# Kernel tuning notes

Hardware: AMD Instinct MI355X
Metric: run time of the kernel (lower is better)

## Reference

```python
import jax, jax.numpy as jnp
import numpy as np
import math

# dims
B, T, D = 2, 1024, 1024
HQ, HKV, KD, VD = 16, 4, 64, 64   # query heads, kv heads, key dim, value dim
G = HQ // HKV                      # query group size
E, TOPK, CAP_FRAC, HID = 8, 2, 0.5, 2048
BASE = 10000.0
EPS = 1e-6


def setup_inputs() -> dict:
    key = jax.random.key(0)
    ks = jax.random.split(key, 12)
    s = jnp.float32(0.02)
    return {
        'x': jax.random.normal(ks[0], (B, T, D), jnp.float32),
        'wq': jax.random.normal(ks[1], (D, KD * HQ), jnp.float32) * s,
        'wk': jax.random.normal(ks[2], (D, KD * HKV), jnp.float32) * s,
        'wv': jax.random.normal(ks[3], (D, VD * HKV), jnp.float32) * s,
        'wo': jax.random.normal(ks[4], (G * HKV * VD, D), jnp.float32) * s,
        'router_w': jax.random.normal(ks[5], (D, E), jnp.float32) * s,
        'router_b': jax.random.normal(ks[6], (E,), jnp.float32) * s,
        'w1': jax.random.normal(ks[7], (E, D, HID), jnp.float32) * s,
        'w2': jax.random.normal(ks[8], (E, D, HID), jnp.float32) * s,
        'w3': jax.random.normal(ks[9], (E, HID, D), jnp.float32) * s,
        'norm1_scale': jnp.ones((D,), jnp.float32),
        'norm2_scale': jnp.ones((D,), jnp.float32),
    }


def _rms(x, scale):
    return x * jax.lax.rsqrt(jnp.mean(x * x, axis=-1, keepdims=True) + EPS) * scale


def _rope(x):
    # x: (B, t, H, d); rotary per RotaryEmbedding: tile(ticks,(1,2)), neg-half rotation
    t, d = x.shape[1], x.shape[3]
    thetas = BASE ** (-jnp.arange(0, d, 2, dtype=jnp.float32) / d)
    ticks = jnp.outer(jnp.arange(t, dtype=jnp.float32), thetas)
    ticks = jnp.tile(ticks, (1, 2))[None, :, None, :]
    cos, sin = jnp.cos(ticks).astype(x.dtype), jnp.sin(ticks).astype(x.dtype)
    x1, x2 = jnp.split(x, 2, axis=-1)
    neg = jnp.concatenate([-x2, x1], axis=-1)
    return x * cos + neg * sin


def reference(x, wq, wk, wv, wo, router_w, router_b, w1, w2, w3, norm1_scale, norm2_scale):
    b, t, d = x.shape
    # ---- pre-norm grouped-query attention with rotary, causal ----
    h = _rms(x, norm1_scale)
    q = (h @ wq).reshape(b, t, HQ, KD)
    k = (h @ wk).reshape(b, t, HKV, KD)
    v = (h @ wv).reshape(b, t, HKV, VD)
    q = _rope(q)
    k = _rope(k)
    qg = q.reshape(b, t, HKV, G, KD)
    scores = jnp.einsum('bthgk,bshk->bhgts', qg, k) / jnp.sqrt(jnp.asarray(KD, x.dtype))
    causal = jnp.tril(jnp.ones((t, t), bool))
    scores = jnp.where(causal, scores, jnp.asarray(-1e9, scores.dtype))
    probs = jax.nn.softmax(scores, axis=-1)
    attn = jnp.einsum('bhgts,bshv->bthgv', probs, v).reshape(b, t, HQ * VD)
    x = x + attn @ wo
    # ---- pre-norm top-k MoE feed-forward (capacity-masked dispatch/combine) ----
    h2 = _rms(x, norm2_scale)
    xf = h2.reshape(b * t, d)
    logits = xf.astype(jnp.float32) @ router_w + router_b        # router in fp32
    gate, assign = jax.lax.top_k(logits, TOPK)                   # (N,k)
    gate = jax.nn.softmax(gate, axis=-1).astype(x.dtype)
    cap = math.floor(b * t * CAP_FRAC)
    onehot = jax.nn.one_hot(assign, E, dtype=jnp.float32)        # (N,k,E)
    pos = jnp.cumsum(jnp.cumsum(onehot, axis=0), axis=1).astype(jnp.int32)
    mask = onehot * (pos < cap)                                  # capacity mask
    token_mask = jnp.sum(mask, axis=-1)                          # (N,k)
    choices = jnp.sum(jax.nn.one_hot(pos, cap, dtype=jnp.float32) * mask[..., None], axis=1)  # (N,E,cap)
    choices = choices.transpose(1, 2, 0)                         # (E,cap,N)
    exp_idx = jnp.einsum('tke,e->tk', mask, jnp.arange(E, dtype=jnp.float32)).astype(jnp.int32)
    pos_idx = jnp.einsum('tke,tke->tk', mask, pos.astype(jnp.float32)).astype(jnp.int32)
    grouped = jnp.einsum('ect,tD->ecD', choices.astype(x.dtype), xf)  # dispatch: (E,cap,D)
    # gated FF per expert: act(w2(x) * w1(x)) @ w3
    hh = jax.nn.gelu(jnp.einsum('ecd,edh->ech', grouped, w2) * jnp.einsum('ecd,edh->ech', grouped, w1))
    eout = jnp.einsum('ech,ehd->ecd', hh, w3)                    # (E,cap,D)
    gathered = eout[exp_idx, pos_idx].reshape(b, t, TOPK, d)
    tm = token_mask.reshape(b, t, TOPK)
    moe = jnp.where(tm[..., None] != 0, gathered, h2[:, :, None, :])  # dropped tokens fall back to input
    moe = jnp.einsum('btkD,btk->btD', moe, gate.reshape(b, t, TOPK))
    return x + moe
```

## Files before the change

### kernel.cpp

```cpp
#include <hip/hip_runtime.h>
#include <math.h>

#define Dm 1024
#define Tn 1024
#define Bn 2
#define NTOK 2048
#define HQn 16
#define HKVn 4
#define KDn 64
#define VDn 64
#define Gn 4
#define NE 8
#define CAPn 1024
#define HIDn 2048
#define QKVS 1536

using frag_ab = __attribute__((ext_vector_type(8))) short;
using f32x4  = __attribute__((ext_vector_type(4))) float;

__device__ __forceinline__ unsigned short f2bf(float f) {
    union { float f; unsigned int u; } v; v.f = f;
    unsigned int r = v.u + 0x7FFFu + ((v.u >> 16) & 1u);
    return (unsigned short)(r >> 16);
}
__device__ __forceinline__ float bf2f(unsigned short b) {
    union { unsigned int u; float f; } v; v.u = ((unsigned int)b) << 16;
    return v.f;
}
__device__ __forceinline__ float gelu_fast(float y) {
    float z = 0.7978845608028654f * (y + 0.044715f * y * y * y);
    float az = fabsf(z);
    float t = __expf(-2.f * az);
    float th = (1.f - t) / (1.f + t);
    th = copysignf(th, z);
    return 0.5f * y * (1.f + th);
}

__global__ void rmsnorm_bf16_kernel(const float* __restrict__ x, const float* __restrict__ scale,
                                    unsigned short* __restrict__ out) {
    int row = blockIdx.x;
    const float* xr = x + (size_t)row * Dm;
    float ss = 0.f;
    for (int d = threadIdx.x; d < Dm; d += 256) { float v = xr[d]; ss += v * v; }
    __shared__ float red[256];
    red[threadIdx.x] = ss; __syncthreads();
    for (int s = 128; s > 0; s >>= 1) {
        if (threadIdx.x < s) red[threadIdx.x] += red[threadIdx.x + s];
        __syncthreads();
    }
    float inv = rsqrtf(red[0] * (1.f / Dm) + 1e-6f);
    for (int d = threadIdx.x; d < Dm; d += 256)
        out[(size_t)row * Dm + d] = f2bf(xr[d] * inv * scale[d]);
}

__global__ void rmsnorm_router_kernel(const float* __restrict__ x2, const float* __restrict__ scale,
                                      const float* __restrict__ rw, const float* __restrict__ rb,
                                      float* __restrict__ h2, int* __restrict__ assign,
                                      float* __restrict__ gate) {
    int row = blockIdx.x;
    const float* xr = x2 + (size_t)row * Dm;
    __shared__ float red[256];
    __shared__ float rowbuf[Dm];
    __shared__ float logits[NE];
    float v4[4]; float ss = 0.f;
    #pragma unroll
    for (int i = 0; i < 4; ++i) { v4[i] = xr[threadIdx.x + 256 * i]; ss += v4[i] * v4[i]; }
    red[threadIdx.x] = ss; __syncthreads();
    for (int s = 128; s > 0; s >>= 1) {
        if (threadIdx.x < s) red[threadIdx.x] += red[threadIdx.x + s];
        __syncthreads();
    }
    float inv = rsqrtf(red[0] * (1.f / Dm) + 1e-6f);
    #pragma unroll
    for (int i = 0; i < 4; ++i) {
        int d = threadIdx.x + 256 * i;
        float h = v4[i] * inv * scale[d];
        h2[(size_t)row * Dm + d] = h;
        rowbuf[d] = h;
    }
    __syncthreads();
    int e = threadIdx.x >> 5, lane32 = threadIdx.x & 31;
    float part = 0.f;
    for (int d = lane32; d < Dm; d += 32) part += rowbuf[d] * rw[(size_t)d * NE + e];
    for (int off = 16; off; off >>= 1) part += __shfl_down(part, off, 32);
    if (lane32 == 0) logits[e] = part + rb[e];
    __syncthreads();
    if (threadIdx.x == 0) {
        int i0 = 0; float m0 = logits[0];
        for (int i = 1; i < NE; ++i) if (logits[i] > m0) { m0 = logits[i]; i0 = i; }
        int i1 = -1; float m1 = -1e30f;
        for (int i = 0; i < NE; ++i) if (i != i0 && logits[i] > m1) { m1 = logits[i]; i1 = i; }
        float e1 = __expf(m1 - m0);
        float s = 1.f + e1;
        assign[row * 2] = i0; assign[row * 2 + 1] = i1;
        gate[row * 2] = 1.f / s; gate[row * 2 + 1] = e1 / s;
    }
}

__global__ void transpose_convert(const float* __restrict__ in, unsigned short* __restrict__ out,
                                  int R, int Ccols) {
    int e = blockIdx.z;
    in  += (size_t)e * R * Ccols;
    out += (size_t)e * R * Ccols;
    __shared__ float T[64][65];
    int tid = threadIdx.x;
    int r0 = blockIdx.y * 64, c0 = blockIdx.x * 64;
    #pragma unroll
    for (int rep = 0; rep < 4; ++rep) {
        int r = (tid >> 4) + rep * 16;
        int c = (tid & 15) * 4;
        float4 v = *(const float4*)(in + (size_t)(r0 + r) * Ccols + c0 + c);
        T[r][c] = v.x; T[r][c + 1] = v.y; T[r][c + 2] = v.z; T[r][c + 3] = v.w;
    }
    __syncthreads();
    #pragma unroll
    for (int rep = 0; rep < 4; ++rep) {
        int c = rep * 16 + (tid >> 4);
        int r = (tid & 15) * 4;
        unsigned long long pk = (unsigned long long)f2bf(T[r][c])
                              | ((unsigned long long)f2bf(T[r + 1][c]) << 16)
                              | ((unsigned long long)f2bf(T[r + 2][c]) << 32)
                              | ((unsigned long long)f2bf(T[r + 3][c]) << 48);
        *(unsigned long long*)(out + (size_t)(c0 + c) * R + r0 + r) = pk;
    }
}

template<int MODE>
__global__ __launch_bounds__(256) void mfma_gemm2(const unsigned short* __restrict__ A,
                                                  const unsigned short* __restrict__ Bt,
                                                  void* __restrict__ Cout,
                                                  const float* __restrict__ R,
                                                  int N, int K) {
    int m0 = blockIdx.y * 128, n0 = blockIdx.x * 128;
    __shared__ unsigned short As[128 * 32];
    __shared__ unsigned short Bs[128 * 32];
    int tid = threadIdx.x, wave = tid >> 6, lane = tid & 63;
    int quad = lane >> 4, r16 = lane & 15;
    int wm = wave & 1, wn = wave >> 1;
    f32x4 acc[4][4];
    #pragma unroll
    for (int mt = 0; mt < 4; ++mt)
        #pragma unroll
        for (int nt = 0; nt < 4; ++nt) acc[mt][nt] = (f32x4){0.f, 0.f, 0.f, 0.f};
    const size_t rs = (size_t)K * 2;
    const char* ga0 = (const char*)A  + (size_t)m0 * rs;
    const char* gb0 = (const char*)Bt + (size_t)n0 * rs;
    for (int kk = 0; kk < K; kk += 32) {
        __syncthreads();
        #pragma unroll
        for (int i = 0; i < 2; ++i) {
            int r = wave * 16 + i * 64 + (lane >> 2);
            size_t go = (size_t)r * rs + (size_t)kk * 2 + (lane & 3) * 16;
            int lofs = wave * 1024 + i * 4096;
            __builtin_amdgcn_global_load_lds(
                (const __attribute__((address_space(1))) void*)(ga0 + go),
                (__attribute__((address_space(3))) void*)((char*)As + lofs), 16, 0, 0);
            __builtin_amdgcn_global_load_lds(
                (const __attribute__((address_space(1))) void*)(gb0 + go),
                (__attribute__((address_space(3))) void*)((char*)Bs + lofs), 16, 0, 0);
        }
        __syncthreads();
        frag_ab a[4], b[4];
        #pragma unroll
        for (int t = 0; t < 4; ++t) {
            a[t] = *(const frag_ab*)((const char*)As + (wm * 64 + t * 16 + r16) * 64 + quad * 16);
            b[t] = *(const frag_ab*)((const char*)Bs + (wn * 64 + t * 16 + r16) * 64 + quad * 16);
        }
        #pragma unroll
        for (int mt = 0; mt < 4; ++mt)
            #pragma unroll
            for (int nt = 0; nt < 4; ++nt)
                acc[mt][nt] = __builtin_amdgcn_mfma_f32_16x16x32_bf16(a[mt], b[nt], acc[mt][nt], 0, 0, 0);
    }
    #pragma unroll
    for (int mt = 0; mt < 4; ++mt)
        #pragma unroll
        for (int nt = 0; nt < 4; ++nt)
            #pragma unroll
            for (int r = 0; r < 4; ++r) {
                int m = m0 + wm * 64 + mt * 16 + quad * 4 + r;
                int n = n0 + wn * 64 + nt * 16 + r16;
                size_t idx = (size_t)m * N + n;
                float v = acc[mt][nt][r];
                if (MODE == 0) ((unsigned short*)Cout)[idx] = f2bf(v);
                else           ((float*)Cout)[idx] = v + R[idx];
            }
}

__global__ void rope_bf16(unsigned short* __restrict__ p) {
    int idx = blockIdx.x * 256 + threadIdx.x;
    const int QC = NTOK * HQn * 32;
    int i, col, row; float scale;
    if (idx < QC) {
        i = idx & 31; int h = (idx >> 5) & 15; row = idx >> 9;
        col = h * 64 + i; scale = 0.18033688011112042f;
    } else {
        int r = idx - QC;
        i = r & 31; int h = (r >> 5) & 3; row = r >> 7;
        col = 1024 + h * 64 + i; scale = 1.f;
    }
    int t = row & (Tn - 1);
    size_t base = (size_t)row * QKVS + col;
    float theta = __expf(-(float)i * (1.f / 32.f) * 9.210340371976184f);
    float ang = (float)t * theta;
    float c = cosf(ang), s = sinf(ang);
    float x1 = bf2f(p[base]), x2 = bf2f(p[base + 32]);
    p[base]      = f2bf((x1 * c - x2 * s) * scale);
    p[base + 32] = f2bf((x2 * c + x1 * s) * scale);
}

__global__ __launch_bounds__(256) void mfma_attn(const unsigned short* __restrict__ qkv,
                                                 unsigned short* __restrict__ attnb) {
    __shared__ unsigned short lds[32768];
    unsigned short* Ps = lds;
    unsigned short* Ks = lds + 16384;
    unsigned short* Vt = lds + 24576;
    int tid = threadIdx.x, wave = tid >> 6, lane = tid & 63;
    int quad = lane >> 4, r16 = lane & 15;
    int tq0 = blockIdx.x * 128, h = blockIdx.y, b = blockIdx.z;
    int kvh = h >> 2;
    const size_t rowb = QKVS * 2;

    {
        const char* qb = (const char*)(qkv + (size_t)(b * Tn + tq0) * QKVS + h * 64);
        int rloc = lane >> 3, ch = (lane & 7) ^ rloc;
        #pragma unroll
        for (int i = 0; i < 4; ++i) {
            int r0 = wave * 8 + i * 32;
            __builtin_amdgcn_global_load_lds(
                (const __attribute__((address_space(1))) void*)(qb + (size_t)(r0 + rloc) * rowb + ch * 16),
                (__attribute__((address_space(3))) void*)((char*)Vt + r0 * 128), 16, 0, 0);
        }
    }
    __syncthreads();
    frag_ab qf[2][2];
    #pragma unroll
    for (int mt = 0; mt < 2; ++mt)
        #pragma unroll
        for (int ks = 0; ks < 2; ++ks) {
            int m = wave * 32 + mt * 16 + r16;
            int ch = (ks * 4 + quad) ^ (m & 7);
            qf[mt][ks] = *(const frag_ab*)((const char*)Vt + m * 128 + ch * 16);
        }

    float m_i[2][4], l_i[2][4];
    f32x4 O[2][4];
    #pragma unroll
    for (int mt = 0; mt < 2; ++mt) {
        #pragma unroll
        for (int r = 0; r < 4; ++r) { m_i[mt][r] = -1e30f; l_i[mt][r] = 0.f; }
        #pragma unroll
        for (int nt = 0; nt < 4; ++nt) O[mt][nt] = (f32x4){0.f, 0.f, 0.f, 0.f};
    }

    int nst = blockIdx.x + 1;
    for (int st = 0; st < nst; ++st) {
        int s0 = st * 128;
        __syncthreads();
        {
            const char* kb = (const char*)(qkv + (size_t)(b * Tn + s0) * QKVS + 1024 + kvh * 64);
            int rloc = lane >> 3, ch = (lane & 7) ^ rloc;
            #pragma unroll
            for (int i = 0; i < 4; ++i) {
                int r0 = wave * 8 + i * 32;
                __builtin_amdgcn_global_load_lds(
                    (const __attribute__((address_space(1))) void*)(kb + (size_t)(r0 + rloc) * rowb + ch * 16),
                    (__attribute__((address_space(3))) void*)((char*)Ks + r0 * 128), 16, 0, 0);
            }
        }
        {
            const unsigned short* vb = qkv + (size_t)(b * Tn + s0) * QKVS + 1280 + kvh * 64;
            int d4 = (tid & 15) * 4;
            #pragma unroll
            for (int pass = 0; pass < 4; ++pass) {
                int sl = 8 * wave + 2 * (lane >> 4) + pass * 32;
                ushort4 v0 = *(const ushort4*)(vb + (size_t)sl * QKVS + d4);
                ushort4 v1 = *(const ushort4*)(vb + (size_t)(sl + 1) * QKVS + d4);
                unsigned short a0[4] = {v0.x, v0.y, v0.z, v0.w};
                unsigned short a1[4] = {v1.x, v1.y, v1.z, v1.w};
                #pragma unroll
                for (int i = 0; i < 4; ++i) {
                    int d = d4 + i;
                    int col = (((sl >> 3) ^ (d & 15)) << 3) | (sl & 7);
                    *(unsigned int*)(Vt + d * 128 + col) =
                        (unsigned int)a0[i] | ((unsigned int)a1[i] << 16);
                }
            }
        }
        __syncthreads();
        f32x4 Sacc[2][8];
        #pragma unroll
        for (int mt = 0; mt < 2; ++mt)
            #pragma unroll
            for (int nt = 0; nt < 8; ++nt) Sacc[mt][nt] = (f32x4){0.f, 0.f, 0.f, 0.f};
        #pragma unroll
        for (int ks = 0; ks < 2; ++ks) {
            frag_ab kf[8];
            #pragma unroll
            for (int nt = 0; nt < 8; ++nt) {
                int n = nt * 16 + r16;
                int ch = (ks * 4 + quad) ^ (n & 7);
                kf[nt] = *(const frag_ab*)((const char*)Ks + n * 128 + ch * 16);
            }
            #pragma unroll
            for (int mt = 0; mt < 2; ++mt)
                #pragma unroll
                for (int nt = 0; nt < 8; ++nt)
                    Sacc[mt][nt] = __builtin_amdgcn_mfma_f32_16x16x32_bf16(qf[mt][ks], kf[nt], Sacc[mt][nt], 0, 0, 0);
        }
        if (st == nst - 1) {
            #pragma unroll
            for (int mt = 0; mt < 2; ++mt) {
                int trow = wave * 32 + mt * 16 + quad * 4;
                #pragma unroll
                for (int nt = 0; nt < 8; ++nt) {
                    int scol = nt * 16 + r16;
                    #pragma unroll
                    for (int r = 0; r < 4; ++r)
                        if (scol > trow + r) Sacc[mt][nt][r] = -1e30f;
                }
            }
        }
        #pragma unroll
        for (int mt = 0; mt < 2; ++mt) {
            float mx[4];
            #pragma unroll
            for (int r = 0; r < 4; ++r) {
                float m_ = Sacc[mt][0][r];
                #pragma unroll
                for (int nt = 1; nt < 8; ++nt) m_ = fmaxf(m_, Sacc[mt][nt][r]);
                mx[r] = m_;
            }
            #pragma unroll
            for (int off = 1; off < 16; off <<= 1)
                #pragma unroll
                for (int r = 0; r < 4; ++r) mx[r] = fmaxf(mx[r], __shfl_xor(mx[r], off));
            #pragma unroll
            for (int r = 0; r < 4; ++r) {
                float mn = fmaxf(m_i[mt][r], mx[r]);
                float al = exp2f(m_i[mt][r] - mn);
                m_i[mt][r] = mn;
                l_i[mt][r] *= al;
                #pragma unroll
                for (int nt = 0; nt < 4; ++nt) O[mt][nt][r] *= al;
            }
            float rsum[4] = {0.f, 0.f, 0.f, 0.f};
            #pragma unroll
            for (int nt = 0; nt < 8; ++nt)
                #pragma unroll
                for (int r = 0; r < 4; ++r) {
                    float pv = exp2f(Sacc[mt][nt][r] - m_i[mt][r]);
                    Sacc[mt][nt][r] = pv;
                    rsum[r] += pv;
                }
            #pragma unroll
            for (int off = 1; off < 16; off <<= 1)
                #pragma unroll
                for (int r = 0; r < 4; ++r) rsum[r] += __shfl_xor(rsum[r], off);
            #pragma unroll
            for (int r = 0; r < 4; ++r) l_i[mt][r] += rsum[r];
            #pragma unroll
            for (int nt = 0; nt < 8; ++nt) {
                int scol = nt * 16 + r16;
                int chb = scol >> 3;
                #pragma unroll
                for (int r = 0; r < 4; ++r) {
                    int m = wave * 32 + mt * 16 + quad * 4 + r;
                    int col = ((chb ^ (m & 15)) << 3) | (scol & 7);
                    Ps[m * 128 + col] = f2bf(Sacc[mt][nt][r]);
                }
            }
        }
        #pragma unroll
        for (int ks = 0; ks < 4; ++ks) {
            frag_ab pa[2], vf[4];
            #pragma unroll
            for (int mt = 0; mt < 2; ++mt) {
                int m = wave * 32 + mt * 16 + r16;
                int ch = (ks * 4 + quad) ^ (m & 15);
                pa[mt] = *(const frag_ab*)((const char*)Ps + m * 256 + ch * 16);
            }
            #pragma unroll
            for (int nt = 0; nt < 4; ++nt) {
                int n = nt * 16 + r16;
                int ch = (ks * 4 + quad) ^ (n & 15);
                vf[nt] = *(const frag_ab*)((const char*)Vt + n * 256 + ch * 16);
            }
            #pragma unroll
            for (int mt = 0; mt < 2; ++mt)
                #pragma unroll
                for (int nt = 0; nt < 4; ++nt)
                    O[mt][nt] = __builtin_amdgcn_mfma_f32_16x16x32_bf16(pa[mt], vf[nt], O[mt][nt], 0, 0, 0);
        }
    }
    #pragma unroll
    for (int mt = 0; mt < 2; ++mt) {
        float inv[4];
        #pragma unroll
        for (int r = 0; r < 4; ++r) inv[r] = 1.f / l_i[mt][r];
        #pragma unroll
        for (int nt = 0; nt < 4; ++nt)
            #pragma unroll
            for (int r = 0; r < 4; ++r) {
                int t = tq0 + wave * 32 + mt * 16 + quad * 4 + r;
                int c = h * 64 + nt * 16 + r16;
                attnb[(size_t)(b * Tn + t) * Dm + c] = f2bf(O[mt][nt][r] * inv[r]);
            }
    }
}

__global__ void scan_kernel(const int* __restrict__ assign, int* __restrict__ pos,
                            int* __restrict__ limit) {
    __shared__ int cnt[256][16];
    __shared__ int tot[16];
    int tid = threadIdx.x;
    int local[16];
    #pragma unroll
    for (int i = 0; i < 16; ++i) local[i] = 0;
    for (int r = 0; r < 8; ++r) {
        int t = tid * 8 + r;
        local[assign[t * 2]]++;
        local[8 + assign[t * 2 + 1]]++;
    }
    #pragma unroll
    for (int i = 0; i < 16; ++i) cnt[tid][i] = local[i];
    __syncthreads();
    if (tid < 16) {
        int run = 0;
        for (int th = 0; th < 256; ++th) { int v = cnt[th][tid]; cnt[th][tid] = run; run += v; }
        tot[tid] = run;
    }
    __syncthreads();
    int r0[NE], r1[NE];
    #pragma unroll
    for (int e = 0; e < NE; ++e) { r0[e] = cnt[tid][e]; r1[e] = cnt[tid][8 + e]; }
    for (int r = 0; r < 8; ++r) {
        int t = tid * 8 + r;
        int e0 = assign[t * 2], e1 = assign[t * 2 + 1];
        r0[e0]++; pos[t * 2] = r0[e0];
        r1[e1]++; pos[t * 2 + 1] = r0[e1] + r1[e1];
    }
    if (tid == 0)
        for (int e = 0; e < NE; ++e) {
            int C = tot[e] + tot[8 + e];
            limit[e] = C < (CAPn - 1) ? C : (CAPn - 1);
        }
}

__global__ void dispatch_kernel(const float* __restrict__ h2, const int* __restrict__ assign,
                                const int* __restrict__ pos, float* __restrict__ grouped) {
    int slot = blockIdx.x;
    int p = pos[slot];
    if (p >= CAPn) return;
    int e = assign[slot];
    const float* src = h2 + (size_t)(slot >> 1) * Dm;
    float* dst = grouped + ((size_t)e * CAPn + p) * Dm;
    for (int d = threadIdx.x; d < Dm; d += 256) atomicAdd(&dst[d], src[d]);
}

__global__ void convert_bf16(const float* __restrict__ in, unsigned short* __restrict__ out, int n4) {
    int i = blockIdx.x * 256 + threadIdx.x;
    if (i >= n4) return;
    float4 v = ((const float4*)in)[i];
    unsigned long long pk = (unsigned long long)f2bf(v.x)
                          | ((unsigned long long)f2bf(v.y) << 16)
                          | ((unsigned long long)f2bf(v.z) << 32)
                          | ((unsigned long long)f2bf(v.w) << 48);
    ((unsigned long long*)out)[i] = pk;
}

template<bool GELU>
__global__ __launch_bounds__(256) void mfma_gemm(const unsigned short* __restrict__ A,
                                                 const unsigned short* __restrict__ Bt,
                                                 unsigned short* __restrict__ C,
                                                 int N, int K, const int* __restrict__ limit) {
    int e = blockIdx.z;
    int m0 = blockIdx.y * 128;
    if (m0 > limit[e]) return;
    A  += (size_t)e * CAPn * K;
    Bt += (size_t)e * N * K;
    C  += (size_t)e * CAPn * N;
    int n0 = blockIdx.x * 128;
    __shared__ unsigned short As[128 * 32];
    __shared__ unsigned short Bs[128 * 32];
    int tid = threadIdx.x, wave = tid >> 6, lane = tid & 63;
    int quad = lane >> 4, r16 = lane & 15;
    int wm = wave & 1, wn = wave >> 1;
    f32x4 acc[4][4];
    #pragma unroll
    for (int mt = 0; mt < 4; ++mt)
        #pragma unroll
        for (int nt = 0; nt < 4; ++nt) acc[mt][nt] = (f32x4){0.f, 0.f, 0.f, 0.f};
    const size_t rs = (size_t)K * 2;
    const char* ga0 = (const char*)A  + (size_t)m0 * rs;
    const char* gb0 = (const char*)Bt + (size_t)n0 * rs;
    for (int kk = 0; kk < K; kk += 32) {
        __syncthreads();
        #pragma unroll
        for (int i = 0; i < 2; ++i) {
            int r = wave * 16 + i * 64 + (lane >> 2);
            size_t go = (size_t)r * rs + (size_t)kk * 2 + (lane & 3) * 16;
            int lofs = wave * 1024 + i * 4096;
            __builtin_amdgcn_global_load_lds(
                (const __attribute__((address_space(1))) void*)(ga0 + go),
                (__attribute__((address_space(3))) void*)((char*)As + lofs), 16, 0, 0);
            __builtin_amdgcn_global_load_lds(
                (const __attribute__((address_space(1))) void*)(gb0 + go),
                (__attribute__((address_space(3))) void*)((char*)Bs + lofs), 16, 0, 0);
        }
        __syncthreads();
        frag_ab a[4], b[4];
        #pragma unroll
        for (int t = 0; t < 4; ++t) {
            a[t] = *(const frag_ab*)((const char*)As + (wm * 64 + t * 16 + r16) * 64 + quad * 16);
            b[t] = *(const frag_ab*)((const char*)Bs + (wn * 64 + t * 16 + r16) * 64 + quad * 16);
        }
        #pragma unroll
        for (int mt = 0; mt < 4; ++mt)
            #pragma unroll
            for (int nt = 0; nt < 4; ++nt)
                acc[mt][nt] = __builtin_amdgcn_mfma_f32_16x16x32_bf16(a[mt], b[nt], acc[mt][nt], 0, 0, 0);
    }
    #pragma unroll
    for (int mt = 0; mt < 4; ++mt)
        #pragma unroll
        for (int nt = 0; nt < 4; ++nt)
            #pragma unroll
            for (int r = 0; r < 4; ++r) {
                int m = m0 + wm * 64 + mt * 16 + quad * 4 + r;
                int n = n0 + wn * 64 + nt * 16 + r16;
                size_t idx = (size_t)m * N + n;
                float v = acc[mt][nt][r];
                if (GELU) v = gelu_fast(v * bf2f(C[idx]));
                C[idx] = f2bf(v);
            }
}

__global__ void combine_kernel(const float* __restrict__ x2, const float* __restrict__ h2,
                               const unsigned short* __restrict__ eout, const int* __restrict__ assign,
                               const int* __restrict__ pos, const float* __restrict__ gate,
                               float* __restrict__ out) {
    int t = blockIdx.x;
    int e0 = assign[t * 2], e1 = assign[t * 2 + 1];
    int p0 = pos[t * 2],   p1 = pos[t * 2 + 1];
    float g0 = gate[t * 2], g1 = gate[t * 2 + 1];
    bool k0 = p0 < CAPn, k1 = p1 < CAPn;
    const unsigned short* s0 = eout + ((size_t)e0 * CAPn + p0) * Dm;
    const unsigned short* s1 = eout + ((size_t)e1 * CAPn + p1) * Dm;
    const float* hb = h2 + (size_t)t * Dm;
    for (int d = threadIdx.x; d < Dm; d += 256) {
        float v0 = k0 ? bf2f(s0[d]) : hb[d];
        float v1 = k1 ? bf2f(s1[d]) : hb[d];
        out[(size_t)t * Dm + d] = x2[(size_t)t * Dm + d] + g0 * v0 + g1 * v1;
    }
}

extern "C" void kernel_launch(void* const* d_in, const int* in_sizes, int n_in,
                              void* d_out, int out_size, void* d_ws, size_t ws_size,
                              hipStream_t stream) {
    const float* x        = (const float*)d_in[0];
    const float* wq       = (const float*)d_in[1];
    const float* wk       = (const float*)d_in[2];
    const float* wv       = (const float*)d_in[3];
    const float* wo       = (const float*)d_in[4];
    const float* router_w = (const float*)d_in[5];
    const float* router_b = (const float*)d_in[6];
    const float* w1       = (const float*)d_in[7];
    const float* w2       = (const float*)d_in[8];
    const float* w3       = (const float*)d_in[9];
    const float* n1s      = (const float*)d_in[10];
    const float* n2s      = (const float*)d_in[11];
    float* out = (float*)d_out;
    unsigned char* ws = (unsigned char*)d_ws;
    const size_t MB = 1ull << 20;

    unsigned short* h_bf  = (unsigned short*)(ws + 0 * MB);
    unsigned short* qkv   = (unsigned short*)(ws + 4 * MB);
    unsigned short* wqkvt = (unsigned short*)(ws + 10 * MB);
    unsigned short* attnb = (unsigned short*)(ws + 13 * MB);
    unsigned short* wot   = (unsigned short*)(ws + 17 * MB);
    float* grouped_f32    = (float*)(ws + 0 * MB);
    unsigned short* tmp1hh = (unsigned short*)(ws + 0 * MB);
    float* x2      = (float*)(ws + 32 * MB);
    float* h2      = (float*)(ws + 40 * MB);
    int*   assign  = (int*)  (ws + 48 * MB);
    int*   pos     = (int*)  (ws + 48 * MB + 65536);
    float* gate    = (float*)(ws + 48 * MB + 131072);
    int*   limit   = (int*)  (ws + 48 * MB + 196608);
    unsigned short* grouped_bf = (unsigned short*)(ws + 49 * MB);
    unsigned short* wtslot     = (unsigned short*)(ws + 65 * MB);
    unsigned short* eout       = (unsigned short*)(ws + 97 * MB);
    (void)in_sizes; (void)n_in; (void)out_size; (void)ws_size;

    transpose_convert<<<dim3(16, 16, 1), 256, 0, stream>>>(wq, wqkvt, Dm, Dm);
    transpose_convert<<<dim3(4, 16, 1), 256, 0, stream>>>(wk, wqkvt + 1024 * 1024, Dm, 256);
    transpose_convert<<<dim3(4, 16, 1), 256, 0, stream>>>(wv, wqkvt + 1280 * 1024, Dm, 256);
    transpose_convert<<<dim3(16, 16, 1), 256, 0, stream>>>(wo, wot, Dm, Dm);
    rmsnorm_bf16_kernel<<<NTOK, 256, 0, stream>>>(x, n1s, h_bf);
    mfma_gemm2<0><<<dim3(QKVS / 128, NTOK / 128), 256, 0, stream>>>(h_bf, wqkvt, qkv, nullptr, QKVS, Dm);
    rope_bf16<<<(NTOK * (HQn + HKVn) * 32) / 256, 256, 0, stream>>>(qkv);
    mfma_attn<<<dim3(Tn / 128, HQn, Bn), 256, 0, stream>>>(qkv, attnb);
    mfma_gemm2<1><<<dim3(Dm / 128, NTOK / 128), 256, 0, stream>>>(attnb, wot, x2, x, Dm, Dm);
    rmsnorm_router_kernel<<<NTOK, 256, 0, stream>>>(x2, n2s, router_w, router_b, h2, assign, gate);
    scan_kernel<<<1, 256, 0, stream>>>(assign, pos, limit);
    hipMemsetAsync(grouped_f32, 0, (size_t)NE * CAPn * Dm * sizeof(float), stream);
    dispatch_kernel<<<NTOK * 2, 256, 0, stream>>>(h2, assign, pos, grouped_f32);
    convert_bf16<<<(NE * CAPn * Dm / 4 + 255) / 256, 256, 0, stream>>>(grouped_f32, grouped_bf, NE * CAPn * Dm / 4);
    transpose_convert<<<dim3(HIDn / 64, Dm / 64, NE), 256, 0, stream>>>(w1, wtslot, Dm, HIDn);
    mfma_gemm<false><<<dim3(HIDn / 128, CAPn / 128, NE), 256, 0, stream>>>(grouped_bf, wtslot, tmp1hh, HIDn, Dm, limit);
    transpose_convert<<<dim3(HIDn / 64, Dm / 64, NE), 256, 0, stream>>>(w2, wtslot, Dm, HIDn);
    mfma_gemm<true><<<dim3(HIDn / 128, CAPn / 128, NE), 256, 0, stream>>>(grouped_bf, wtslot, tmp1hh, HIDn, Dm, limit);
    transpose_convert<<<dim3(Dm / 64, HIDn / 64, NE), 256, 0, stream>>>(w3, wtslot, HIDn, Dm);
    mfma_gemm<false><<<dim3(Dm / 128, CAPn / 128, NE), 256, 0, stream>>>(tmp1hh, wtslot, eout, Dm, HIDn, limit);
    combine_kernel<<<NTOK, 256, 0, stream>>>(x2, h2, eout, assign, pos, gate, out);
}
```

Before: 566.1 us.

## Fuse w1/w2 expert GEMMs with gelu epilogue, swizzle LDS, convert grouped in place

The two expert up-projections are merged into one GEMM. Rows of w1 and w2 are interleaved in the B tile, so each pair of adjacent accumulator columns gives w2*w1, which is gated through gelu in the epilogue via a lane shuffle. This replaces the separate w1 GEMM, the read-back of its result, and the second GEMM pass. The hidden dimension is split into two halves to fit the workspace, and the w3 GEMM reads both halves and uses a 64-wide N tile. The grouped activations are converted to bf16 in place, removing a separate buffer, and an XOR swizzle is applied to LDS writes and reads to reduce bank conflicts in all MFMA GEMMs.

```diff
diff --git a/kernel.cpp b/kernel.cpp
--- a/kernel.cpp
+++ b/kernel.cpp
@@ -35,6 +35,10 @@
     th = copysignf(th, z);
     return 0.5f * y * (1.f + th);
 }
+
+#define GLOAD16(gp, lp) __builtin_amdgcn_global_load_lds( \
+    (const __attribute__((address_space(1))) void*)(gp), \
+    (__attribute__((address_space(3))) void*)(lp), 16, 0, 0)
 
 __global__ void rmsnorm_bf16_kernel(const float* __restrict__ x, const float* __restrict__ scale,
                                     unsigned short* __restrict__ out) {
@@ -98,10 +102,11 @@
 }
 
 __global__ void transpose_convert(const float* __restrict__ in, unsigned short* __restrict__ out,
-                                  int R, int Ccols) {
+                                  int R, int Cstride, int c_base) {
     int e = blockIdx.z;
-    in  += (size_t)e * R * Ccols;
-    out += (size_t)e * R * Ccols;
+    int Cext = gridDim.x * 64;
+    in  += (size_t)e * R * Cstride;
+    out += (size_t)e * R * Cext;
     __shared__ float T[64][65];
     int tid = threadIdx.x;
     int r0 = blockIdx.y * 64, c0 = blockIdx.x * 64;
@@ -109,7 +114,7 @@
     for (int rep = 0; rep < 4; ++rep) {
         int r = (tid >> 4) + rep * 16;
         int c = (tid & 15) * 4;
-        float4 v = *(const float4*)(in + (size_t)(r0 + r) * Ccols + c0 + c);
+        float4 v = *(const float4*)(in + (size_t)(r0 + r) * Cstride + c_base + c0 + c);
         T[r][c] = v.x; T[r][c + 1] = v.y; T[r][c + 2] = v.z; T[r][c + 3] = v.w;
     }
     __syncthreads();
@@ -137,6 +142,8 @@
     int tid = threadIdx.x, wave = tid >> 6, lane = tid & 63;
     int quad = lane >> 4, r16 = lane & 15;
     int wm = wave & 1, wn = wave >> 1;
+    int ch16 = ((lane & 3) ^ ((lane >> 3) & 3)) * 16;
+    int rofs = (quad ^ ((r16 >> 1) & 3)) * 16;
     f32x4 acc[4][4];
     #pragma unroll
     for (int mt = 0; mt < 4; ++mt)
@@ -150,21 +157,17 @@
         #pragma unroll
         for (int i = 0; i < 2; ++i) {
             int r = wave * 16 + i * 64 + (lane >> 2);
-            size_t go = (size_t)r * rs + (size_t)kk * 2 + (lane & 3) * 16;
+            size_t go = (size_t)r * rs + (size_t)kk * 2 + ch16;
             int lofs = wave * 1024 + i * 4096;
-            __builtin_amdgcn_global_load_lds(
-                (const __attribute__((address_space(1))) void*)(ga0 + go),
-                (__attribute__((address_space(3))) void*)((char*)As + lofs), 16, 0, 0);
-            __builtin_amdgcn_global_load_lds(
-                (const __attribute__((address_space(1))) void*)(gb0 + go),
-                (__attribute__((address_space(3))) void*)((char*)Bs + lofs), 16, 0, 0);
+            GLOAD16(ga0 + go, (char*)As + lofs);
+            GLOAD16(gb0 + go, (char*)Bs + lofs);
         }
         __syncthreads();
         frag_ab a[4], b[4];
         #pragma unroll
         for (int t = 0; t < 4; ++t) {
-            a[t] = *(const frag_ab*)((const char*)As + (wm * 64 + t * 16 + r16) * 64 + quad * 16);
-            b[t] = *(const frag_ab*)((const char*)Bs + (wn * 64 + t * 16 + r16) * 64 + quad * 16);
+            a[t] = *(const frag_ab*)((const char*)As + (wm * 64 + t * 16 + r16) * 64 + rofs);
+            b[t] = *(const frag_ab*)((const char*)Bs + (wn * 64 + t * 16 + r16) * 64 + rofs);
         }
         #pragma unroll
         for (int mt = 0; mt < 4; ++mt)
@@ -458,62 +461,59 @@
     for (int d = threadIdx.x; d < Dm; d += 256) atomicAdd(&dst[d], src[d]);
 }
 
-__global__ void convert_bf16(const float* __restrict__ in, unsigned short* __restrict__ out, int n4) {
-    int i = blockIdx.x * 256 + threadIdx.x;
-    if (i >= n4) return;
-    float4 v = ((const float4*)in)[i];
+__global__ void convert_inplace(float* __restrict__ buf) {
+    float* rp = buf + (size_t)blockIdx.x * Dm;
+    float4 v = ((const float4*)rp)[threadIdx.x];
+    __syncthreads();
     unsigned long long pk = (unsigned long long)f2bf(v.x)
                           | ((unsigned long long)f2bf(v.y) << 16)
                           | ((unsigned long long)f2bf(v.z) << 32)
                           | ((unsigned long long)f2bf(v.w) << 48);
-    ((unsigned long long*)out)[i] = pk;
-}
-
-template<bool GELU>
-__global__ __launch_bounds__(256) void mfma_gemm(const unsigned short* __restrict__ A,
-                                                 const unsigned short* __restrict__ Bt,
-                                                 unsigned short* __restrict__ C,
-                                                 int N, int K, const int* __restrict__ limit) {
+    ((unsigned long long*)rp)[threadIdx.x] = pk;
+}
+
+__global__ __launch_bounds__(256) void mfma_gemm_fused(const float* __restrict__ grouped,
+                                                       const unsigned short* __restrict__ B1t,
+                                                       const unsigned short* __restrict__ B2t,
+                                                       unsigned short* __restrict__ hh,
+                                                       const int* __restrict__ limit) {
     int e = blockIdx.z;
     int m0 = blockIdx.y * 128;
     if (m0 > limit[e]) return;
-    A  += (size_t)e * CAPn * K;
-    Bt += (size_t)e * N * K;
-    C  += (size_t)e * CAPn * N;
     int n0 = blockIdx.x * 128;
+    const char* ga0 = (const char*)grouped + ((size_t)e * CAPn + m0) * 4096;
+    const unsigned short* b1 = B1t + (size_t)e * 1024 * Dm;
+    const unsigned short* b2 = B2t + (size_t)e * 1024 * Dm;
+    unsigned short* Ch = hh + (size_t)e * CAPn * 1024;
     __shared__ unsigned short As[128 * 32];
     __shared__ unsigned short Bs[128 * 32];
     int tid = threadIdx.x, wave = tid >> 6, lane = tid & 63;
     int quad = lane >> 4, r16 = lane & 15;
     int wm = wave & 1, wn = wave >> 1;
+    int ch16 = ((lane & 3) ^ ((lane >> 3) & 3)) * 16;
+    int rofs = (quad ^ ((r16 >> 1) & 3)) * 16;
     f32x4 acc[4][4];
     #pragma unroll
     for (int mt = 0; mt < 4; ++mt)
         #pragma unroll
         for (int nt = 0; nt < 4; ++nt) acc[mt][nt] = (f32x4){0.f, 0.f, 0.f, 0.f};
-    const size_t rs = (size_t)K * 2;
-    const char* ga0 = (const char*)A  + (size_t)m0 * rs;
-    const char* gb0 = (const char*)Bt + (size_t)n0 * rs;
-    for (int kk = 0; kk < K; kk += 32) {
+    for (int kk = 0; kk < Dm; kk += 32) {
         __syncthreads();
         #pragma unroll
         for (int i = 0; i < 2; ++i) {
             int r = wave * 16 + i * 64 + (lane >> 2);
-            size_t go = (size_t)r * rs + (size_t)kk * 2 + (lane & 3) * 16;
             int lofs = wave * 1024 + i * 4096;
-            __builtin_amdgcn_global_load_lds(
-                (const __attribute__((address_space(1))) void*)(ga0 + go),
-                (__attribute__((address_space(3))) void*)((char*)As + lofs), 16, 0, 0);
-            __builtin_amdgcn_global_load_lds(
-                (const __attribute__((address_space(1))) void*)(gb0 + go),
-                (__attribute__((address_space(3))) void*)((char*)Bs + lofs), 16, 0, 0);
+            GLOAD16(ga0 + (size_t)r * 4096 + (size_t)kk * 2 + ch16, (char*)As + lofs);
+            const unsigned short* bb = (r & 1) ? b2 : b1;
+            size_t go = (size_t)((n0 + r) >> 1) * 2048 + (size_t)kk * 2 + ch16;
+            GLOAD16((const char*)bb + go, (char*)Bs + lofs);
         }
         __syncthreads();
         frag_ab a[4], b[4];
         #pragma unroll
         for (int t = 0; t < 4; ++t) {
-            a[t] = *(const frag_ab*)((const char*)As + (wm * 64 + t * 16 + r16) * 64 + quad * 16);
-            b[t] = *(const frag_ab*)((const char*)Bs + (wn * 64 + t * 16 + r16) * 64 + quad * 16);
+            a[t] = *(const frag_ab*)((const char*)As + (wm * 64 + t * 16 + r16) * 64 + rofs);
+            b[t] = *(const frag_ab*)((const char*)Bs + (wn * 64 + t * 16 + r16) * 64 + rofs);
         }
         #pragma unroll
         for (int mt = 0; mt < 4; ++mt)
@@ -527,12 +527,77 @@
         for (int nt = 0; nt < 4; ++nt)
             #pragma unroll
             for (int r = 0; r < 4; ++r) {
+                float v = acc[mt][nt][r];
+                float w = __shfl_xor(v, 1);
+                if (!(r16 & 1)) {
+                    int m = m0 + wm * 64 + mt * 16 + quad * 4 + r;
+                    int j = (n0 + wn * 64 + nt * 16 + r16) >> 1;
+                    Ch[(size_t)m * 1024 + j] = f2bf(gelu_fast(v * w));
+                }
+            }
+}
+
+__global__ __launch_bounds__(256) void mfma_gemm_w3(const unsigned short* __restrict__ hhA,
+                                                    const unsigned short* __restrict__ hhB,
+                                                    const unsigned short* __restrict__ Bt,
+                                                    unsigned short* __restrict__ C,
+                                                    const int* __restrict__ limit) {
+    int e = blockIdx.z;
+    int m0 = blockIdx.y * 128;
+    if (m0 > limit[e]) return;
+    int n0 = blockIdx.x * 64;
+    const char* gaA = (const char*)hhA + ((size_t)e * CAPn + m0) * 2048;
+    const char* gaB = (const char*)hhB + ((size_t)e * CAPn + m0) * 2048;
+    const char* gb0 = (const char*)Bt + ((size_t)e * 1024 + n0) * 4096;
+    C += (size_t)e * CAPn * 1024;
+    __shared__ unsigned short As[128 * 32];
+    __shared__ unsigned short Bs[64 * 32];
+    int tid = threadIdx.x, wave = tid >> 6, lane = tid & 63;
+    int quad = lane >> 4, r16 = lane & 15;
+    int wm = wave & 1, wn = wave >> 1;
+    int ch16 = ((lane & 3) ^ ((lane >> 3) & 3)) * 16;
+    int rofs = (quad ^ ((r16 >> 1) & 3)) * 16;
+    f32x4 acc[4][2];
+    #pragma unroll
+    for (int mt = 0; mt < 4; ++mt)
+        #pragma unroll
+        for (int nt = 0; nt < 2; ++nt) acc[mt][nt] = (f32x4){0.f, 0.f, 0.f, 0.f};
+    for (int kk = 0; kk < HIDn; kk += 32) {
+        const char* ga = (kk < 1024) ? gaA : gaB;
+        size_t kb = (size_t)(kk & 1023) * 2;
+        __syncthreads();
+        #pragma unroll
+        for (int i = 0; i < 2; ++i) {
+            int r = wave * 16 + i * 64 + (lane >> 2);
+            GLOAD16(ga + (size_t)r * 2048 + kb + ch16, (char*)As + wave * 1024 + i * 4096);
+        }
+        {
+            int r = wave * 16 + (lane >> 2);
+            GLOAD16(gb0 + (size_t)r * 4096 + (size_t)kk * 2 + ch16, (char*)Bs + wave * 1024);
+        }
+        __syncthreads();
+        frag_ab a[4], b[2];
+        #pragma unroll
+        for (int t = 0; t < 4; ++t)
+            a[t] = *(const frag_ab*)((const char*)As + (wm * 64 + t * 16 + r16) * 64 + rofs);
+        #pragma unroll
+        for (int t = 0; t < 2; ++t)
+            b[t] = *(const frag_ab*)((const char*)Bs + (wn * 32 + t * 16 + r16) * 64 + rofs);
+        #pragma unroll
+        for (int mt = 0; mt < 4; ++mt)
+            #pragma unroll
+            for (int nt = 0; nt < 2; ++nt)
+                acc[mt][nt] = __builtin_amdgcn_mfma_f32_16x16x32_bf16(a[mt], b[nt], acc[mt][nt], 0, 0, 0);
+    }
+    #pragma unroll
+    for (int mt = 0; mt < 4; ++mt)
+        #pragma unroll
+        for (int nt = 0; nt < 2; ++nt)
+            #pragma unroll
+            for (int r = 0; r < 4; ++r) {
                 int m = m0 + wm * 64 + mt * 16 + quad * 4 + r;
-                int n = n0 + wn * 64 + nt * 16 + r16;
-                size_t idx = (size_t)m * N + n;
-                float v = acc[mt][nt][r];
-                if (GELU) v = gelu_fast(v * bf2f(C[idx]));
-                C[idx] = f2bf(v);
+                int n = n0 + wn * 32 + nt * 16 + r16;
+                C[(size_t)m * 1024 + n] = f2bf(acc[mt][nt][r]);
             }
 }
 
@@ -580,22 +645,24 @@
     unsigned short* attnb = (unsigned short*)(ws + 13 * MB);
     unsigned short* wot   = (unsigned short*)(ws + 17 * MB);
     float* grouped_f32    = (float*)(ws + 0 * MB);
-    unsigned short* tmp1hh = (unsigned short*)(ws + 0 * MB);
+    unsigned short* eout  = (unsigned short*)(ws + 0 * MB);
     float* x2      = (float*)(ws + 32 * MB);
     float* h2      = (float*)(ws + 40 * MB);
     int*   assign  = (int*)  (ws + 48 * MB);
     int*   pos     = (int*)  (ws + 48 * MB + 65536);
     float* gate    = (float*)(ws + 48 * MB + 131072);
     int*   limit   = (int*)  (ws + 48 * MB + 196608);
-    unsigned short* grouped_bf = (unsigned short*)(ws + 49 * MB);
-    unsigned short* wtslot     = (unsigned short*)(ws + 65 * MB);
-    unsigned short* eout       = (unsigned short*)(ws + 97 * MB);
+    unsigned short* wtA = (unsigned short*)(ws + 49 * MB);
+    unsigned short* wtB = (unsigned short*)(ws + 65 * MB);
+    unsigned short* wt3 = (unsigned short*)(ws + 49 * MB);
+    unsigned short* hhA = (unsigned short*)(ws + 81 * MB);
+    unsigned short* hhB = (unsigned short*)(ws + 97 * MB);
     (void)in_sizes; (void)n_in; (void)out_size; (void)ws_size;
 
-    transpose_convert<<<dim3(16, 16, 1), 256, 0, stream>>>(wq, wqkvt, Dm, Dm);
-    transpose_convert<<<dim3(4, 16, 1), 256, 0, stream>>>(wk, wqkvt + 1024 * 1024, Dm, 256);
-    transpose_convert<<<dim3(4, 16, 1), 256, 0, stream>>>(wv, wqkvt + 1280 * 1024, Dm, 256);
-    transpose_convert<<<dim3(16, 16, 1), 256, 0, stream>>>(wo, wot, Dm, Dm);
+    transpose_convert<<<dim3(16, 16, 1), 256, 0, stream>>>(wq, wqkvt, Dm, Dm, 0);
+    transpose_convert<<<dim3(4, 16, 1), 256, 0, stream>>>(wk, wqkvt + 1024 * 1024, Dm, 256, 0);
+    transpose_convert<<<dim3(4, 16, 1), 256, 0, stream>>>(wv, wqkvt + 1280 * 1024, Dm, 256, 0);
+    transpose_convert<<<dim3(16, 16, 1), 256, 0, stream>>>(wo, wot, Dm, Dm, 0);
     rmsnorm_bf16_kernel<<<NTOK, 256, 0, stream>>>(x, n1s, h_bf);
     mfma_gemm2<0><<<dim3(QKVS / 128, NTOK / 128), 256, 0, stream>>>(h_bf, wqkvt, qkv, nullptr, QKVS, Dm);
     rope_bf16<<<(NTOK * (HQn + HKVn) * 32) / 256, 256, 0, stream>>>(qkv);
@@ -605,12 +672,14 @@
     scan_kernel<<<1, 256, 0, stream>>>(assign, pos, limit);
     hipMemsetAsync(grouped_f32, 0, (size_t)NE * CAPn * Dm * sizeof(float), stream);
     dispatch_kernel<<<NTOK * 2, 256, 0, stream>>>(h2, assign, pos, grouped_f32);
-    convert_bf16<<<(NE * CAPn * Dm / 4 + 255) / 256, 256, 0, stream>>>(grouped_f32, grouped_bf, NE * CAPn * Dm / 4);
-    transpose_convert<<<dim3(HIDn / 64, Dm / 64, NE), 256, 0, stream>>>(w1, wtslot, Dm, HIDn);
-    mfma_gemm<false><<<dim3(HIDn / 128, CAPn / 128, NE), 256, 0, stream>>>(grouped_bf, wtslot, tmp1hh, HIDn, Dm, limit);
-    transpose_convert<<<dim3(HIDn / 64, Dm / 64, NE), 256, 0, stream>>>(w2, wtslot, Dm, HIDn);
-    mfma_gemm<true><<<dim3(HIDn / 128, CAPn / 128, NE), 256, 0, stream>>>(grouped_bf, wtslot, tmp1hh, HIDn, Dm, limit);
-    transpose_convert<<<dim3(Dm / 64, HIDn / 64, NE), 256, 0, stream>>>(w3, wtslot, HIDn, Dm);
-    mfma_gemm<false><<<dim3(Dm / 128, CAPn / 128, NE), 256, 0, stream>>>(tmp1hh, wtslot, eout, Dm, HIDn, limit);
+    convert_inplace<<<NE * CAPn, 256, 0, stream>>>(grouped_f32);
+    transpose_convert<<<dim3(16, 16, NE), 256, 0, stream>>>(w1, wtA, Dm, HIDn, 0);
+    transpose_convert<<<dim3(16, 16, NE), 256, 0, stream>>>(w2, wtB, Dm, HIDn, 0);
+    mfma_gemm_fused<<<dim3(16, CAPn / 128, NE), 256, 0, stream>>>(grouped_f32, wtA, wtB, hhA, limit);
+    transpose_convert<<<dim3(16, 16, NE), 256, 0, stream>>>(w1, wtA, Dm, HIDn, 1024);
+    transpose_convert<<<dim3(16, 16, NE), 256, 0, stream>>>(w2, wtB, Dm, HIDn, 1024);
+    mfma_gemm_fused<<<dim3(16, CAPn / 128, NE), 256, 0, stream>>>(grouped_f32, wtA, wtB, hhB, limit);
+    transpose_convert<<<dim3(16, 32, NE), 256, 0, stream>>>(w3, wt3, HIDn, Dm, 0);
+    mfma_gemm_w3<<<dim3(16, CAPn / 128, NE), 256, 0, stream>>>(hhA, hhB, wt3, eout, limit);
     combine_kernel<<<NTOK, 256, 0, stream>>>(x2, h2, eout, assign, pos, gate, out);
 }
```

After: 561.5 us. No clear change (-0.8%).
